# Performance work log

Measured on AMD Instinct MI355X. Metric: run time of the kernel, lower is better.

## Reference

```python
import jax, jax.numpy as jnp
import numpy as np

EPS = 1e-6


def _norm(v):
    # L2 norm over last axis
    return jnp.linalg.norm(v, axis=-1)


def _dot(a, b):
    return jnp.sum(a * b, axis=-1)


def _cross2(a, b):
    # z-component of 2D cross product (intended math of torch.cross on 2D points)
    return a[..., 0] * b[..., 1] - a[..., 1] * b[..., 0]


def _quad_area(p1, p2, p3, p4):
    area1 = 0.5 * jnp.abs(_cross2(p2 - p1, p3 - p1))
    area2 = 0.5 * jnp.abs(_cross2(p3 - p1, p4 - p1))
    return area1 + area2


def setup_inputs() -> dict:
    key = jax.random.key(0)
    k1, k2 = jax.random.split(key)
    B, K = 524288, 8
    pred_kpts = jax.random.uniform(k1, (B, K, 3), dtype=jnp.float32)
    gt_kpts = jax.random.uniform(k2, (B, K, 3), dtype=jnp.float32)
    return {"pred_kpts": pred_kpts, "gt_kpts": gt_kpts}


def reference(pred_kpts, gt_kpts):
    # visibility: both pred and gt z-score > 0.5
    visible = (pred_kpts[..., 2] > 0.5) & (gt_kpts[..., 2] > 0.5)  # [B, K]

    # compact: indices of first 4 visible keypoints per sample (stable sort
    # puts visible indices first, preserving original order)
    order = jnp.argsort(jnp.logical_not(visible), axis=1, stable=True)  # [B, K]
    idx = order[:, :4]                                                   # [B, 4]
    pc = jnp.take_along_axis(pred_kpts[..., :2], idx[:, :, None], axis=1)  # [B,4,2]
    gc = jnp.take_along_axis(gt_kpts[..., :2], idx[:, :, None], axis=1)   # [B,4,2]

    valid = jnp.sum(visible, axis=1) >= 4  # [B]

    p1, p2, p3, p4 = pc[:, 0], pc[:, 1], pc[:, 2], pc[:, 3]
    g1, g2, g3, g4 = gc[:, 0], gc[:, 1], gc[:, 2], gc[:, 3]

    # --- L_shape: diagonal cross-ratio consistency ---
    pred_cr = _norm(p3 - p1) / (_norm(p4 - p2) + EPS)
    gt_cr = _norm(g3 - g1) / (_norm(g4 - g2) + EPS)
    L_shape = jnp.abs(pred_cr - gt_cr)

    # --- L_edge: parallelism + perpendicularity of predicted quad ---
    v12, v23, v34, v41 = p2 - p1, p3 - p2, p4 - p3, p1 - p4
    l12, l23, l34, l41 = _norm(v12), _norm(v23), _norm(v34), _norm(v41)
    par1 = jnp.abs(l12 - l34) / (l12 + l34 + EPS)
    par2 = jnp.abs(l23 - l41) / (l23 + l41 + EPS)
    dot1 = jnp.abs(_dot(v12, v41) / (l12 * l41 + EPS))
    dot2 = jnp.abs(_dot(v12, v23) / (l12 * l23 + EPS))
    dot3 = jnp.abs(_dot(v23, v34) / (l23 * l34 + EPS))
    dot4 = jnp.abs(_dot(v34, v41) / (l34 * l41 + EPS))
    L_edge = (par1 + par2) * 0.5 + (dot1 + dot2 + dot3 + dot4) * 0.25

    # --- L_position: dist + area ratio + relative-position consistency ---
    dist = jnp.mean(_norm(pc - gc), axis=-1)
    pred_area = _quad_area(p1, p2, p3, p4)
    gt_area = _quad_area(g1, g2, g3, g4)
    area_ratio = jnp.abs(pred_area - gt_area) / (gt_area + EPS)
    pred_rel = pc - jnp.mean(pc, axis=1, keepdims=True)
    gt_rel = gc - jnp.mean(gc, axis=1, keepdims=True)
    rel_cons = jnp.mean(_norm(pred_rel - gt_rel), axis=-1)
    L_pos = 0.4 * dist + 0.3 * area_ratio + 0.3 * rel_cons

    L = 0.4 * L_shape + 0.3 * L_edge + 0.3 * L_pos  # [B]

    n_valid = jnp.sum(valid)
    total = jnp.sum(jnp.where(valid, L, 0.0))
    return jnp.where(n_valid > 0,
                     total / jnp.maximum(n_valid, 1).astype(L.dtype),
                     jnp.zeros((), dtype=L.dtype))
```

## Files before the change

kernel.cpp:

```cpp
#include <hip/hip_runtime.h>

#define EPS 1e-6f
#define NT  256

__device__ __forceinline__ float norm2f(float dx, float dy) {
    return sqrtf(dx * dx + dy * dy);
}

__device__ __forceinline__ float sel8s(int k, float v0, float v1, float v2,
                                       float v3, float v4, float v5, float v6,
                                       float v7) {
    float r = v0;
    r = (k == 1) ? v1 : r;
    r = (k == 2) ? v2 : r;
    r = (k == 3) ? v3 : r;
    r = (k == 4) ? v4 : r;
    r = (k == 5) ? v5 : r;
    r = (k == 6) ? v6 : r;
    r = (k == 7) ? v7 : r;
    return r;
}

__global__ __launch_bounds__(256) void gsc_loss_kernel(
    const float* __restrict__ pred, const float* __restrict__ gt,
    float2* __restrict__ partials, int B)
{
    __shared__ float4 sT[NT * 7];
    const int t = threadIdx.x;
    const size_t rowBase = (size_t)blockIdx.x * NT;

    const float4* p4 = reinterpret_cast<const float4*>(pred) + rowBase * 6;
    const float4* g4 = reinterpret_cast<const float4*>(gt)   + rowBase * 6;
    float4 pr0 = p4[t + 0 * NT], pr1 = p4[t + 1 * NT], pr2 = p4[t + 2 * NT];
    float4 pr3 = p4[t + 3 * NT], pr4 = p4[t + 4 * NT], pr5 = p4[t + 5 * NT];
    float4 gr0 = g4[t + 0 * NT], gr1 = g4[t + 1 * NT], gr2 = g4[t + 2 * NT];
    float4 gr3 = g4[t + 3 * NT], gr4 = g4[t + 4 * NT], gr5 = g4[t + 5 * NT];

#define SLOT(i) (7 * ((t + (i) * NT) / 6) + ((t + (i) * NT) % 6))
    sT[SLOT(0)] = pr0; sT[SLOT(1)] = pr1; sT[SLOT(2)] = pr2;
    sT[SLOT(3)] = pr3; sT[SLOT(4)] = pr4; sT[SLOT(5)] = pr5;
    __syncthreads();
    float4 pA = sT[t * 7 + 0], pB = sT[t * 7 + 1], pC = sT[t * 7 + 2];
    float4 pD = sT[t * 7 + 3], pE = sT[t * 7 + 4], pF = sT[t * 7 + 5];

    float px0 = pA.x, py0 = pA.y, pz0 = pA.z;
    float px1 = pA.w, py1 = pB.x, pz1 = pB.y;
    float px2 = pB.z, py2 = pB.w, pz2 = pC.x;
    float px3 = pC.y, py3 = pC.z, pz3 = pC.w;
    float px4 = pD.x, py4 = pD.y, pz4 = pD.z;
    float px5 = pD.w, py5 = pE.x, pz5 = pE.y;
    float px6 = pE.z, py6 = pE.w, pz6 = pF.x;
    float px7 = pF.y, py7 = pF.z, pz7 = pF.w;
    __syncthreads();

    sT[SLOT(0)] = gr0; sT[SLOT(1)] = gr1; sT[SLOT(2)] = gr2;
    sT[SLOT(3)] = gr3; sT[SLOT(4)] = gr4; sT[SLOT(5)] = gr5;
#undef SLOT
    __syncthreads();
    float4 gA = sT[t * 7 + 0], gB = sT[t * 7 + 1], gC = sT[t * 7 + 2];
    float4 gD = sT[t * 7 + 3], gE = sT[t * 7 + 4], gF = sT[t * 7 + 5];

    float gx0 = gA.x, gy0 = gA.y, gz0 = gA.z;
    float gx1 = gA.w, gy1 = gB.x, gz1 = gB.y;
    float gx2 = gB.z, gy2 = gB.w, gz2 = gC.x;
    float gx3 = gC.y, gy3 = gC.z, gz3 = gC.w;
    float gx4 = gD.x, gy4 = gD.y, gz4 = gD.z;
    float gx5 = gD.w, gy5 = gE.x, gz5 = gE.y;
    float gx6 = gE.z, gy6 = gE.w, gz6 = gF.x;
    float gx7 = gF.y, gy7 = gF.z, gz7 = gF.w;

    float L = 0.0f, vflag = 0.0f;

    unsigned mask = 0;
    mask |= (pz0 > 0.5f && gz0 > 0.5f) ? 1u   : 0u;
    mask |= (pz1 > 0.5f && gz1 > 0.5f) ? 2u   : 0u;
    mask |= (pz2 > 0.5f && gz2 > 0.5f) ? 4u   : 0u;
    mask |= (pz3 > 0.5f && gz3 > 0.5f) ? 8u   : 0u;
    mask |= (pz4 > 0.5f && gz4 > 0.5f) ? 16u  : 0u;
    mask |= (pz5 > 0.5f && gz5 > 0.5f) ? 32u  : 0u;
    mask |= (pz6 > 0.5f && gz6 > 0.5f) ? 64u  : 0u;
    mask |= (pz7 > 0.5f && gz7 > 0.5f) ? 128u : 0u;

    if ((rowBase + t) < (size_t)B && __popc(mask) >= 4) {
        vflag = 1.0f;

        unsigned m = mask;
        int k0 = __ffs(m) - 1; m &= m - 1;
        int k1 = __ffs(m) - 1; m &= m - 1;
        int k2 = __ffs(m) - 1; m &= m - 1;
        int k3 = __ffs(m) - 1;

        float P1x = sel8s(k0, px0, px1, px2, px3, px4, px5, px6, px7);
        float P1y = sel8s(k0, py0, py1, py2, py3, py4, py5, py6, py7);
        float G1x = sel8s(k0, gx0, gx1, gx2, gx3, gx4, gx5, gx6, gx7);
        float G1y = sel8s(k0, gy0, gy1, gy2, gy3, gy4, gy5, gy6, gy7);
        float P2x = sel8s(k1, px0, px1, px2, px3, px4, px5, px6, px7);
        float P2y = sel8s(k1, py0, py1, py2, py3, py4, py5, py6, py7);
        float G2x = sel8s(k1, gx0, gx1, gx2, gx3, gx4, gx5, gx6, gx7);
        float G2y = sel8s(k1, gy0, gy1, gy2, gy3, gy4, gy5, gy6, gy7);
        float P3x = sel8s(k2, px0, px1, px2, px3, px4, px5, px6, px7);
        float P3y = sel8s(k2, py0, py1, py2, py3, py4, py5, py6, py7);
        float G3x = sel8s(k2, gx0, gx1, gx2, gx3, gx4, gx5, gx6, gx7);
        float G3y = sel8s(k2, gy0, gy1, gy2, gy3, gy4, gy5, gy6, gy7);
        float P4x = sel8s(k3, px0, px1, px2, px3, px4, px5, px6, px7);
        float P4y = sel8s(k3, py0, py1, py2, py3, py4, py5, py6, py7);
        float G4x = sel8s(k3, gx0, gx1, gx2, gx3, gx4, gx5, gx6, gx7);
        float G4y = sel8s(k3, gy0, gy1, gy2, gy3, gy4, gy5, gy6, gy7);

        float pd31x = P3x - P1x, pd31y = P3y - P1y;
        float pd42x = P4x - P2x, pd42y = P4y - P2y;
        float gd31x = G3x - G1x, gd31y = G3y - G1y;
        float gd42x = G4x - G2x, gd42y = G4y - G2y;
        float pred_cr = norm2f(pd31x, pd31y) / (norm2f(pd42x, pd42y) + EPS);
        float gt_cr   = norm2f(gd31x, gd31y) / (norm2f(gd42x, gd42y) + EPS);
        float L_shape = fabsf(pred_cr - gt_cr);

        float v12x = P2x - P1x, v12y = P2y - P1y;
        float v23x = P3x - P2x, v23y = P3y - P2y;
        float v34x = P4x - P3x, v34y = P4y - P3y;
        float v41x = P1x - P4x, v41y = P1y - P4y;
        float l12 = norm2f(v12x, v12y), l23 = norm2f(v23x, v23y);
        float l34 = norm2f(v34x, v34y), l41 = norm2f(v41x, v41y);
        float par1 = fabsf(l12 - l34) / (l12 + l34 + EPS);
        float par2 = fabsf(l23 - l41) / (l23 + l41 + EPS);
        float dot1 = fabsf((v12x * v41x + v12y * v41y) / (l12 * l41 + EPS));
        float dot2 = fabsf((v12x * v23x + v12y * v23y) / (l12 * l23 + EPS));
        float dot3 = fabsf((v23x * v34x + v23y * v34y) / (l23 * l34 + EPS));
        float dot4 = fabsf((v34x * v41x + v34y * v41y) / (l34 * l41 + EPS));
        float L_edge = 0.5f * (par1 + par2) + 0.25f * (dot1 + dot2 + dot3 + dot4);

        float dist = 0.25f * (norm2f(P1x - G1x, P1y - G1y) +
                              norm2f(P2x - G2x, P2y - G2y) +
                              norm2f(P3x - G3x, P3y - G3y) +
                              norm2f(P4x - G4x, P4y - G4y));

        float p21x = P2x - P1x, p21y = P2y - P1y;
        float p41x = P4x - P1x, p41y = P4y - P1y;
        float g21x = G2x - G1x, g21y = G2y - G1y;
        float g41x = G4x - G1x, g41y = G4y - G1y;
        float pred_area = 0.5f * fabsf(p21x * pd31y - p21y * pd31x)
                        + 0.5f * fabsf(pd31x * p41y - pd31y * p41x);
        float gt_area   = 0.5f * fabsf(g21x * gd31y - g21y * gd31x)
                        + 0.5f * fabsf(gd31x * g41y - gd31y * g41x);
        float area_ratio = fabsf(pred_area - gt_area) / (gt_area + EPS);

        float mpx = 0.25f * (P1x + P2x + P3x + P4x);
        float mpy = 0.25f * (P1y + P2y + P3y + P4y);
        float mgx = 0.25f * (G1x + G2x + G3x + G4x);
        float mgy = 0.25f * (G1y + G2y + G3y + G4y);
        float rel_cons = 0.25f *
            (norm2f((P1x - mpx) - (G1x - mgx), (P1y - mpy) - (G1y - mgy)) +
             norm2f((P2x - mpx) - (G2x - mgx), (P2y - mpy) - (G2y - mgy)) +
             norm2f((P3x - mpx) - (G3x - mgx), (P3y - mpy) - (G3y - mgy)) +
             norm2f((P4x - mpx) - (G4x - mgx), (P4y - mpy) - (G4y - mgy)));

        float L_pos = 0.4f * dist + 0.3f * area_ratio + 0.3f * rel_cons;
        L = 0.4f * L_shape + 0.3f * L_edge + 0.3f * L_pos;
    }

#pragma unroll
    for (int off = 32; off > 0; off >>= 1) {
        L     += __shfl_down(L, off, 64);
        vflag += __shfl_down(vflag, off, 64);
    }
    __shared__ float sL[4], sV[4];
    int lane = threadIdx.x & 63;
    int wv   = threadIdx.x >> 6;
    if (lane == 0) { sL[wv] = L; sV[wv] = vflag; }
    __syncthreads();
    if (threadIdx.x == 0) {
        float tL = sL[0] + sL[1] + sL[2] + sL[3];
        float tV = sV[0] + sV[1] + sV[2] + sV[3];
        partials[blockIdx.x] = make_float2(tL, tV);
    }
}

__global__ __launch_bounds__(256) void gsc_reduce_kernel(
    const float2* __restrict__ partials, int nPart, float* __restrict__ out)
{
    float sLsum = 0.0f, sVsum = 0.0f;
    for (int i = threadIdx.x; i < nPart; i += 256) {
        float2 p = partials[i];
        sLsum += p.x;
        sVsum += p.y;
    }
#pragma unroll
    for (int off = 32; off > 0; off >>= 1) {
        sLsum += __shfl_down(sLsum, off, 64);
        sVsum += __shfl_down(sVsum, off, 64);
    }
    __shared__ float sL[4], sV[4];
    int lane = threadIdx.x & 63;
    int wv   = threadIdx.x >> 6;
    if (lane == 0) { sL[wv] = sLsum; sV[wv] = sVsum; }
    __syncthreads();
    if (threadIdx.x == 0) {
        float tL = sL[0] + sL[1] + sL[2] + sL[3];
        float tV = sV[0] + sV[1] + sV[2] + sV[3];
        out[0] = (tV > 0.0f) ? (tL / tV) : 0.0f;
    }
}

extern "C" void kernel_launch(void* const* d_in, const int* in_sizes, int n_in,
                              void* d_out, int out_size, void* d_ws, size_t ws_size,
                              hipStream_t stream) {
    const float* pred = (const float*)d_in[0];
    const float* gt   = (const float*)d_in[1];
    float* out = (float*)d_out;
    float2* partials = (float2*)d_ws;

    int B = in_sizes[0] / 24;
    int grid = (B + NT - 1) / NT;

    gsc_loss_kernel<<<grid, NT, 0, stream>>>(pred, gt, partials, B);
    gsc_reduce_kernel<<<1, 256, 0, stream>>>(partials, grid, out);
}
```

Measured before the change: 116.8 us.

## Use single-wave blocks, stage pred and gt together, use fast sqrt/rcp

Shrinks blocks from 256 to 64 threads, so each block is one wavefront. This removes the shared-memory cross-wave reduction, and each wave writes its partial sum directly. The pred and gt tiles are staged into a doubled LDS buffer with a single barrier instead of three. IEEE sqrt and division are replaced with the hardware sqrt and reciprocal-multiply intrinsics to cut ALU cost. The trade-offs are slightly lower precision and four times more partials for the final reduce kernel. It also depends on the host launch using the new block size.

```diff
diff --git a/kernel.cpp b/kernel.cpp
--- a/kernel.cpp
+++ b/kernel.cpp
@@ -1,10 +1,16 @@
 #include <hip/hip_runtime.h>
 
 #define EPS 1e-6f
-#define NT  256
-
+#define NT  64
+
+__device__ __forceinline__ float fsqrt_fast(float x) {
+    return __builtin_amdgcn_sqrtf(x);
+}
+__device__ __forceinline__ float fdiv_fast(float a, float b) {
+    return a * __builtin_amdgcn_rcpf(b);
+}
 __device__ __forceinline__ float norm2f(float dx, float dy) {
-    return sqrtf(dx * dx + dy * dy);
+    return fsqrt_fast(dx * dx + dy * dy);
 }
 
 __device__ __forceinline__ float sel8s(int k, float v0, float v1, float v2,
@@ -21,11 +27,11 @@
     return r;
 }
 
-__global__ __launch_bounds__(256) void gsc_loss_kernel(
+__global__ __launch_bounds__(64) void gsc_loss_kernel(
     const float* __restrict__ pred, const float* __restrict__ gt,
     float2* __restrict__ partials, int B)
 {
-    __shared__ float4 sT[NT * 7];
+    __shared__ float4 sT[NT * 7 * 2];
     const int t = threadIdx.x;
     const size_t rowBase = (size_t)blockIdx.x * NT;
 
@@ -37,11 +43,20 @@
     float4 gr3 = g4[t + 3 * NT], gr4 = g4[t + 4 * NT], gr5 = g4[t + 5 * NT];
 
 #define SLOT(i) (7 * ((t + (i) * NT) / 6) + ((t + (i) * NT) % 6))
-    sT[SLOT(0)] = pr0; sT[SLOT(1)] = pr1; sT[SLOT(2)] = pr2;
-    sT[SLOT(3)] = pr3; sT[SLOT(4)] = pr4; sT[SLOT(5)] = pr5;
+    sT[SLOT(0)]          = pr0; sT[SLOT(1)]          = pr1;
+    sT[SLOT(2)]          = pr2; sT[SLOT(3)]          = pr3;
+    sT[SLOT(4)]          = pr4; sT[SLOT(5)]          = pr5;
+    sT[NT * 7 + SLOT(0)] = gr0; sT[NT * 7 + SLOT(1)] = gr1;
+    sT[NT * 7 + SLOT(2)] = gr2; sT[NT * 7 + SLOT(3)] = gr3;
+    sT[NT * 7 + SLOT(4)] = gr4; sT[NT * 7 + SLOT(5)] = gr5;
+#undef SLOT
     __syncthreads();
+
     float4 pA = sT[t * 7 + 0], pB = sT[t * 7 + 1], pC = sT[t * 7 + 2];
     float4 pD = sT[t * 7 + 3], pE = sT[t * 7 + 4], pF = sT[t * 7 + 5];
+    float4 gA = sT[NT * 7 + t * 7 + 0], gB = sT[NT * 7 + t * 7 + 1];
+    float4 gC = sT[NT * 7 + t * 7 + 2], gD = sT[NT * 7 + t * 7 + 3];
+    float4 gE = sT[NT * 7 + t * 7 + 4], gF = sT[NT * 7 + t * 7 + 5];
 
     float px0 = pA.x, py0 = pA.y, pz0 = pA.z;
     float px1 = pA.w, py1 = pB.x, pz1 = pB.y;
@@ -51,14 +66,6 @@
     float px5 = pD.w, py5 = pE.x, pz5 = pE.y;
     float px6 = pE.z, py6 = pE.w, pz6 = pF.x;
     float px7 = pF.y, py7 = pF.z, pz7 = pF.w;
-    __syncthreads();
-
-    sT[SLOT(0)] = gr0; sT[SLOT(1)] = gr1; sT[SLOT(2)] = gr2;
-    sT[SLOT(3)] = gr3; sT[SLOT(4)] = gr4; sT[SLOT(5)] = gr5;
-#undef SLOT
-    __syncthreads();
-    float4 gA = sT[t * 7 + 0], gB = sT[t * 7 + 1], gC = sT[t * 7 + 2];
-    float4 gD = sT[t * 7 + 3], gE = sT[t * 7 + 4], gF = sT[t * 7 + 5];
 
     float gx0 = gA.x, gy0 = gA.y, gz0 = gA.z;
     float gx1 = gA.w, gy1 = gB.x, gz1 = gB.y;
@@ -111,8 +118,8 @@
         float pd42x = P4x - P2x, pd42y = P4y - P2y;
         float gd31x = G3x - G1x, gd31y = G3y - G1y;
         float gd42x = G4x - G2x, gd42y = G4y - G2y;
-        float pred_cr = norm2f(pd31x, pd31y) / (norm2f(pd42x, pd42y) + EPS);
-        float gt_cr   = norm2f(gd31x, gd31y) / (norm2f(gd42x, gd42y) + EPS);
+        float pred_cr = fdiv_fast(norm2f(pd31x, pd31y), norm2f(pd42x, pd42y) + EPS);
+        float gt_cr   = fdiv_fast(norm2f(gd31x, gd31y), norm2f(gd42x, gd42y) + EPS);
         float L_shape = fabsf(pred_cr - gt_cr);
 
         float v12x = P2x - P1x, v12y = P2y - P1y;
@@ -121,12 +128,12 @@
         float v41x = P1x - P4x, v41y = P1y - P4y;
         float l12 = norm2f(v12x, v12y), l23 = norm2f(v23x, v23y);
         float l34 = norm2f(v34x, v34y), l41 = norm2f(v41x, v41y);
-        float par1 = fabsf(l12 - l34) / (l12 + l34 + EPS);
-        float par2 = fabsf(l23 - l41) / (l23 + l41 + EPS);
-        float dot1 = fabsf((v12x * v41x + v12y * v41y) / (l12 * l41 + EPS));
-        float dot2 = fabsf((v12x * v23x + v12y * v23y) / (l12 * l23 + EPS));
-        float dot3 = fabsf((v23x * v34x + v23y * v34y) / (l23 * l34 + EPS));
-        float dot4 = fabsf((v34x * v41x + v34y * v41y) / (l34 * l41 + EPS));
+        float par1 = fdiv_fast(fabsf(l12 - l34), l12 + l34 + EPS);
+        float par2 = fdiv_fast(fabsf(l23 - l41), l23 + l41 + EPS);
+        float dot1 = fabsf(fdiv_fast(v12x * v41x + v12y * v41y, l12 * l41 + EPS));
+        float dot2 = fabsf(fdiv_fast(v12x * v23x + v12y * v23y, l12 * l23 + EPS));
+        float dot3 = fabsf(fdiv_fast(v23x * v34x + v23y * v34y, l23 * l34 + EPS));
+        float dot4 = fabsf(fdiv_fast(v34x * v41x + v34y * v41y, l34 * l41 + EPS));
         float L_edge = 0.5f * (par1 + par2) + 0.25f * (dot1 + dot2 + dot3 + dot4);
 
         float dist = 0.25f * (norm2f(P1x - G1x, P1y - G1y) +
@@ -142,7 +149,7 @@
                         + 0.5f * fabsf(pd31x * p41y - pd31y * p41x);
         float gt_area   = 0.5f * fabsf(g21x * gd31y - g21y * gd31x)
                         + 0.5f * fabsf(gd31x * g41y - gd31y * g41x);
-        float area_ratio = fabsf(pred_area - gt_area) / (gt_area + EPS);
+        float area_ratio = fdiv_fast(fabsf(pred_area - gt_area), gt_area + EPS);
 
         float mpx = 0.25f * (P1x + P2x + P3x + P4x);
         float mpy = 0.25f * (P1y + P2y + P3y + P4y);
@@ -163,16 +170,7 @@
         L     += __shfl_down(L, off, 64);
         vflag += __shfl_down(vflag, off, 64);
     }
-    __shared__ float sL[4], sV[4];
-    int lane = threadIdx.x & 63;
-    int wv   = threadIdx.x >> 6;
-    if (lane == 0) { sL[wv] = L; sV[wv] = vflag; }
-    __syncthreads();
-    if (threadIdx.x == 0) {
-        float tL = sL[0] + sL[1] + sL[2] + sL[3];
-        float tV = sV[0] + sV[1] + sV[2] + sV[3];
-        partials[blockIdx.x] = make_float2(tL, tV);
-    }
+    if (t == 0) partials[blockIdx.x] = make_float2(L, vflag);
 }
 
 __global__ __launch_bounds__(256) void gsc_reduce_kernel(
```

New measurement: 121.5 us. +4.0%, slower.
